# Performance work log

Hardware: AMD Instinct MI355X
Metric: run time of the kernel (lower is better)

The kernel has to match this reference:

```python
import jax, jax.numpy as jnp
import numpy as np

B, C, L, H = 4, 1024, 2048, 16
D = C // H


def setup_inputs() -> dict:
    key = jax.random.key(0)
    k1, k2, k3, k4 = jax.random.split(key, 4)
    queries = jax.random.normal(k1, (B, C, L), dtype=jnp.float32)
    mask = jax.random.randint(k2, (B, L), 0, 2, dtype=jnp.int32)
    # Conv1d(kernel_size=1, bias=False) weights, stored as [out_ch, in_ch]
    Wm = jax.random.normal(k3, (2 * C, C), dtype=jnp.float32) * (1.0 / np.sqrt(C))
    Wq = jax.random.normal(k4, (C, C), dtype=jnp.float32) * (1.0 / np.sqrt(C))
    return {"queries": queries, "mask": mask, "Wm": Wm, "Wq": Wq}


def reference(queries, mask, Wm, Wq):
    # 1x1 conv == channel-wise linear: [B,C,L] -> [B,L,out]
    mem = jnp.einsum("oc,bcl->blo", Wm, queries)   # [B, L, 2C]
    q = jnp.einsum("oc,bcl->blo", Wq, queries)      # [B, L, C]

    def split_heads(x):  # [B, L, C'] -> [B, H, L, D']
        b, l, c = x.shape
        return x.reshape(b, l, H, c // H).transpose(0, 2, 1, 3)

    Q = split_heads(q) * (D ** -0.5)                # [B, H, L, D]
    K = split_heads(mem[..., :C])                   # [B, H, L, D]
    V = split_heads(mem[..., C:])                   # [B, H, L, D]

    logits = jnp.einsum("bhqd,bhkd->bhqk", Q, K)    # [B, H, L, L]
    m = mask.astype(jnp.float32)[:, None, None, :]  # [B, 1, 1, L]
    NEG_INF = jnp.float32(-1e30)
    logits = logits * m + (1.0 - m) * NEG_INF
    weights = jax.nn.softmax(logits, axis=-1)
    x = jnp.einsum("bhqk,bhkd->bhqd", weights, V)   # [B, H, L, D]
    # combine heads and return [B, C, L]
    out = x.transpose(0, 2, 1, 3).reshape(B, L, C).transpose(0, 2, 1)
    return out
```

## Files before the change

### kernel.cpp

```cpp
#include <hip/hip_runtime.h>


typedef __bf16 bf16x8 __attribute__((ext_vector_type(8)));
typedef float f32x4 __attribute__((ext_vector_type(4)));
typedef float f32x16 __attribute__((ext_vector_type(16)));
typedef unsigned int u32x4 __attribute__((ext_vector_type(4)));

#define MFMA16(a, b, c) __builtin_amdgcn_mfma_f32_16x16x32_bf16((a), (b), (c), 0, 0, 0)
#define MFMA32(a, b, c) __builtin_amdgcn_mfma_f32_32x32x16_bf16((a), (b), (c), 0, 0, 0)

__device__ __forceinline__ unsigned short f2bf(float f) {
  unsigned int u = __float_as_uint(f);
  u += 0x7FFFu + ((u >> 16) & 1u);
  return (unsigned short)(u >> 16);
}

__device__ __forceinline__ void gload16(const void* g, void* lds) {
  __builtin_amdgcn_global_load_lds(
      (const __attribute__((address_space(1))) unsigned int*)g,
      (__attribute__((address_space(3))) unsigned int*)lds, 16, 0, 0);
}


__global__ __launch_bounds__(256) void castw_kernel(const float* __restrict__ Wm,
                                                    const float* __restrict__ Wq,
                                                    unsigned short* __restrict__ Wb) {
  size_t i = ((size_t)blockIdx.x * 256 + threadIdx.x) * 4;
  float4 v;
  if (i < (size_t)2048 * 1024) {
    v = *(const float4*)(Wm + i);
  } else {
    v = *(const float4*)(Wq + (i - (size_t)2048 * 1024));
    const float sc = 0.125f * 1.4426950408889634f;
    v.x *= sc; v.y *= sc; v.z *= sc; v.w *= sc;
  }
  ushort4 o;
  o.x = f2bf(v.x); o.y = f2bf(v.y); o.z = f2bf(v.z); o.w = f2bf(v.w);
  *(ushort4*)(Wb + i) = o;
}

__global__ __launch_bounds__(256) void transq_kernel(const float* __restrict__ q,
                                                     unsigned short* __restrict__ qT) {
  __shared__ float tile[32][33];
  int b = blockIdx.z;
  int l0 = blockIdx.x * 32, c0 = blockIdx.y * 32;
  int tx = threadIdx.x, ty = threadIdx.y;
  const float* src = q + ((size_t)b * 1024 + c0) * 2048 + l0;
#pragma unroll
  for (int i = 0; i < 4; i++)
    tile[ty + i * 8][tx] = src[(size_t)(ty + i * 8) * 2048 + tx];
  __syncthreads();
  unsigned short* dst = qT + ((size_t)b * 2048 + l0) * 1024 + c0;
#pragma unroll
  for (int i = 0; i < 4; i++)
    dst[(size_t)(ty + i * 8) * 1024 + tx] = f2bf(tile[tx][ty + i * 8]);
}

__global__ __launch_bounds__(256) void maskword_kernel(const int* __restrict__ mask,
                                                       unsigned int* __restrict__ mword) {
  int i = blockIdx.x * 256 + threadIdx.x;
  if (i < 4096) {
    const int* mp = mask + i * 2;
    mword[i] = (mp[0] ? 0xFFFFu : 0u) | (mp[1] ? 0xFFFF0000u : 0u);
  }
}


__global__ __launch_bounds__(256) void gemm_kernel(const unsigned short* __restrict__ Wb,
                                                   const unsigned short* __restrict__ qT,
                                                   unsigned short* __restrict__ Kb,
                                                   unsigned short* __restrict__ Vb,
                                                   unsigned short* __restrict__ Qb) {
  __shared__ __align__(16) unsigned short At[128 * 32];
  __shared__ __align__(16) unsigned short Bt[128 * 32];
  int n = blockIdx.x + 16 * (blockIdx.y + 24 * blockIdx.z);
  int lb = (n & 7) * 192 + (n >> 3);
  int bx = lb & 15;
  int by = (lb >> 4) % 24;
  int b = lb / 384;
  int o0 = by * 128, l0 = bx * 128;
  int tid = threadIdx.x, lane = tid & 63, wid = tid >> 6;
  int wr = wid >> 1, wc = wid & 1;
  int ln = lane & 15, g = lane >> 4;

  f32x4 acc[4][4];
#pragma unroll
  for (int m2 = 0; m2 < 4; m2++)
#pragma unroll
    for (int n2 = 0; n2 < 4; n2++) acc[m2][n2] = (f32x4){0.f, 0.f, 0.f, 0.f};

  const unsigned short* wsrc = Wb + (size_t)o0 * 1024;
  const unsigned short* xsrc = qT + ((size_t)b * 2048 + l0) * 1024;
  int c0 = tid, c1 = 256 + tid;

  for (int kk = 0; kk < 1024; kk += 32) {
    gload16(wsrc + (size_t)(c0 >> 2) * 1024 + kk + (c0 & 3) * 8, (char*)At + (size_t)wid * 1024);
    gload16(wsrc + (size_t)(c1 >> 2) * 1024 + kk + (c1 & 3) * 8, (char*)At + 4096 + (size_t)wid * 1024);
    gload16(xsrc + (size_t)(c0 >> 2) * 1024 + kk + (c0 & 3) * 8, (char*)Bt + (size_t)wid * 1024);
    gload16(xsrc + (size_t)(c1 >> 2) * 1024 + kk + (c1 & 3) * 8, (char*)Bt + 4096 + (size_t)wid * 1024);
    __syncthreads();
    bf16x8 af[4], bfv[4];
#pragma unroll
    for (int m2 = 0; m2 < 4; m2++)
      af[m2] = *(const bf16x8*)&At[(wr * 64 + m2 * 16 + ln) * 32 + g * 8];
#pragma unroll
    for (int n2 = 0; n2 < 4; n2++)
      bfv[n2] = *(const bf16x8*)&Bt[(wc * 64 + n2 * 16 + ln) * 32 + g * 8];
#pragma unroll
    for (int m2 = 0; m2 < 4; m2++)
#pragma unroll
      for (int n2 = 0; n2 < 4; n2++)
        acc[m2][n2] = MFMA16(af[m2], bfv[n2], acc[m2][n2]);
    __syncthreads();
  }

  int region = o0 >> 10;
#pragma unroll
  for (int m2 = 0; m2 < 4; m2++) {
    int orow = o0 + wr * 64 + m2 * 16 + g * 4;
#pragma unroll
    for (int n2 = 0; n2 < 4; n2++) {
      int l = l0 + wc * 64 + n2 * 16 + ln;
      if (region == 0) {
        int h = orow >> 6, d = orow & 63;
        ushort4 pk;
        pk.x = f2bf(acc[m2][n2][0]); pk.y = f2bf(acc[m2][n2][1]);
        pk.z = f2bf(acc[m2][n2][2]); pk.w = f2bf(acc[m2][n2][3]);
        *(ushort4*)&Kb[(((size_t)b * 16 + h) * 2048 + l) * 64 + d] = pk;
      } else if (region == 1) {
        int o2 = orow - 1024;
        int h = o2 >> 6, d = o2 & 63;
#pragma unroll
        for (int r = 0; r < 4; r++)
          Vb[(((size_t)b * 16 + h) * 64 + (d + r)) * 2048 + l] = f2bf(acc[m2][n2][r]);
      } else {
        int o2 = orow - 2048;
        int h = o2 >> 6, d = o2 & 63;
        ushort4 pk;
        pk.x = f2bf(acc[m2][n2][0]); pk.y = f2bf(acc[m2][n2][1]);
        pk.z = f2bf(acc[m2][n2][2]); pk.w = f2bf(acc[m2][n2][3]);
        *(ushort4*)&Qb[(((size_t)b * 16 + h) * 2048 + l) * 64 + d] = pk;
      }
    }
  }
}


__global__ __launch_bounds__(256) void attn_kernel(const unsigned short* __restrict__ Kb,
                                                   const unsigned short* __restrict__ Vb,
                                                   const unsigned short* __restrict__ Qb,
                                                   const unsigned int* __restrict__ mword,
                                                   float* __restrict__ out) {
  __shared__ __align__(16) unsigned short Kt[2][4096];
  __shared__ __align__(16) unsigned short Vt[2][4096];

  int n = blockIdx.x;
  int lb = (n & 7) * 128 + (n >> 3);
  int qt = lb & 15;
  int bh = lb >> 4;
  int b = bh >> 4, h = bh & 15;
  int tid = threadIdx.x, lane = tid & 63, w = tid >> 6;
  int c = lane & 31, hi = lane >> 5;
  int q0 = qt * 128 + w * 32;

  const unsigned short* Kp = Kb + (size_t)bh * 2048 * 64;
  const unsigned short* Vp = Vb + (size_t)bh * 2048 * 64;
  const unsigned short* Qp = Qb + (size_t)bh * 2048 * 64;
  const unsigned int* mwp = mword + b * 1024;

  bf16x8 qf[4];
#pragma unroll
  for (int ks = 0; ks < 4; ks++)
    qf[ks] = *(const bf16x8*)&Qp[(size_t)(q0 + c) * 64 + ks * 16 + hi * 8];

  f32x16 Ov0, Ov1, Os;
#pragma unroll
  for (int i = 0; i < 16; i++) { Ov0[i] = 0.f; Ov1[i] = 0.f; Os[i] = 0.f; }

  unsigned int ow = (c == 0) ? 0x3F803F80u : 0u;
  u32x4 ow4 = {ow, ow, ow, ow};
  bf16x8 bones = __builtin_bit_cast(bf16x8, ow4);

  int l8 = (lane & 7) * 16, l3 = lane >> 3;
  int cswz = (c & 7) << 4;

#pragma unroll
  for (int i = 0; i < 2; i++) {
    int widx = w * 2 + i;
    int row = widx * 8 + l3;
    int sb = l8 ^ ((row & 7) << 4);
    gload16((const char*)Kp + (size_t)row * 128 + sb, (char*)Kt[0] + widx * 1024);
    gload16((const char*)Vp + (size_t)row * 4096 + sb, (char*)Vt[0] + widx * 1024);
  }
  __syncthreads();

  for (int kb = 0; kb < 32; kb++) {
    int bs = kb & 1;
    if (kb < 31) {
#pragma unroll
      for (int i = 0; i < 2; i++) {
        int widx = w * 2 + i;
        int row = widx * 8 + l3;
        int sb = l8 ^ ((row & 7) << 4);
        gload16((const char*)Kp + (size_t)(kb * 64 + 64 + row) * 128 + sb,
                (char*)Kt[bs ^ 1] + widx * 1024);
        gload16((const char*)Vp + (size_t)row * 4096 + (kb + 1) * 128 + sb,
                (char*)Vt[bs ^ 1] + widx * 1024);
      }
    }
    u32x4 mw[4];
#pragma unroll
    for (int ks2 = 0; ks2 < 4; ks2++)
      mw[ks2] = *(const u32x4*)(mwp + kb * 32 + ks2 * 8 + hi * 4);

    f32x16 s0, s1;
#pragma unroll
    for (int i = 0; i < 16; i++) { s0[i] = 0.f; s1[i] = 0.f; }
    const char* Kbuf = (const char*)Kt[bs];
    __builtin_amdgcn_s_setprio(1);
#pragma unroll
    for (int ks = 0; ks < 4; ks++) {
      int off = (ks * 32 + hi * 16) ^ cswz;
      bf16x8 a0 = *(const bf16x8*)(Kbuf + c * 128 + off);
      bf16x8 a1 = *(const bf16x8*)(Kbuf + (c + 32) * 128 + off);
      s0 = MFMA32(a0, qf[ks], s0);
      s1 = MFMA32(a1, qf[ks], s1);
    }
    __builtin_amdgcn_s_setprio(0);
#pragma unroll
    for (int i = 0; i < 16; i++) {
      asm("v_exp_f32 %0, %1" : "=v"(s0[i]) : "v"(s0[i]));
      asm("v_exp_f32 %0, %1" : "=v"(s1[i]) : "v"(s1[i]));
    }
    bf16x8 pa[4];
#pragma unroll
    for (int ks2 = 0; ks2 < 4; ks2++) {
      int k1 = (ks2 & 1) * 8;
      unsigned int wds[4];
#pragma unroll
      for (int jj = 0; jj < 2; jj++) {
        unsigned int U, W;
        float u0 = (ks2 < 2) ? s0[k1 + 2 * jj] : s1[k1 + 2 * jj];
        float u1 = (ks2 < 2) ? s0[k1 + 2 * jj + 1] : s1[k1 + 2 * jj + 1];
        float w0 = (ks2 < 2) ? s0[k1 + 4 + 2 * jj] : s1[k1 + 4 + 2 * jj];
        float w1 = (ks2 < 2) ? s0[k1 + 5 + 2 * jj] : s1[k1 + 5 + 2 * jj];
        asm("v_cvt_pk_bf16_f32 %0, %1, %2" : "=v"(U) : "v"(u0), "v"(u1));
        asm("v_cvt_pk_bf16_f32 %0, %1, %2" : "=v"(W) : "v"(w0), "v"(w1));
        asm("v_permlane32_swap_b32 %0, %1" : "+v"(U), "+v"(W));
        wds[jj] = U;
        wds[2 + jj] = W;
      }
      u32x4 wv = {wds[0] & mw[ks2][0], wds[1] & mw[ks2][1],
                  wds[2] & mw[ks2][2], wds[3] & mw[ks2][3]};
      pa[ks2] = __builtin_bit_cast(bf16x8, wv);
    }
    const char* Vbuf = (const char*)Vt[bs];
    __builtin_amdgcn_s_setprio(1);
#pragma unroll
    for (int ks2 = 0; ks2 < 4; ks2++) {
      int off = (ks2 * 32 + hi * 16) ^ cswz;
      bf16x8 v0 = *(const bf16x8*)(Vbuf + c * 128 + off);
      bf16x8 v1 = *(const bf16x8*)(Vbuf + (c + 32) * 128 + off);
      Ov0 = MFMA32(pa[ks2], v0, Ov0);
      Ov1 = MFMA32(pa[ks2], v1, Ov1);
      Os = MFMA32(pa[ks2], bones, Os);
    }
    __builtin_amdgcn_s_setprio(0);
    __syncthreads();
  }

  float rinv[16];
#pragma unroll
  for (int r = 0; r < 16; r++) {
    float d0 = __int_as_float(__builtin_amdgcn_readlane(__float_as_int(Os[r]), 0));
    float d1 = __int_as_float(__builtin_amdgcn_readlane(__float_as_int(Os[r]), 32));
    rinv[r] = __builtin_amdgcn_rcpf(hi ? d1 : d0);
  }

  size_t obase = ((size_t)b * 1024 + h * 64) * 2048 + q0;
#pragma unroll
  for (int g2 = 0; g2 < 4; g2++) {
    int lq = g2 * 8 + hi * 4;
    float4 x0, x1;
    x0.x = Ov0[g2 * 4 + 0] * rinv[g2 * 4 + 0]; x0.y = Ov0[g2 * 4 + 1] * rinv[g2 * 4 + 1];
    x0.z = Ov0[g2 * 4 + 2] * rinv[g2 * 4 + 2]; x0.w = Ov0[g2 * 4 + 3] * rinv[g2 * 4 + 3];
    x1.x = Ov1[g2 * 4 + 0] * rinv[g2 * 4 + 0]; x1.y = Ov1[g2 * 4 + 1] * rinv[g2 * 4 + 1];
    x1.z = Ov1[g2 * 4 + 2] * rinv[g2 * 4 + 2]; x1.w = Ov1[g2 * 4 + 3] * rinv[g2 * 4 + 3];
    *(float4*)(out + obase + (size_t)c * 2048 + lq) = x0;
    *(float4*)(out + obase + (size_t)(32 + c) * 2048 + lq) = x1;
  }
}

extern "C" void kernel_launch(void* const* d_in, const int* in_sizes, int n_in,
                              void* d_out, int out_size, void* d_ws, size_t ws_size,
                              hipStream_t stream) {
  const float* queries = (const float*)d_in[0];
  const int* mask = (const int*)d_in[1];
  const float* Wm = (const float*)d_in[2];
  const float* Wq = (const float*)d_in[3];
  float* out = (float*)d_out;

  char* ws = (char*)d_ws;
  unsigned short* Wb = (unsigned short*)(ws);
  unsigned short* qT = (unsigned short*)(ws + 6291456);
  unsigned short* Kb = (unsigned short*)(ws + 23068672);
  unsigned short* Vb = (unsigned short*)(ws + 39845888);
  unsigned short* Qb = (unsigned short*)(ws + 56623104);
  unsigned int* mwp = (unsigned int*)(ws + 73400320);

  castw_kernel<<<3072, 256, 0, stream>>>(Wm, Wq, Wb);
  transq_kernel<<<dim3(64, 32, 4), dim3(32, 8), 0, stream>>>(queries, qT);
  maskword_kernel<<<16, 256, 0, stream>>>(mask, mwp);
  gemm_kernel<<<dim3(16, 24, 4), 256, 0, stream>>>(Wb, qT, Kb, Vb, Qb);
  attn_kernel<<<1024, 256, 0, stream>>>(Kb, Vb, Qb, mwp, out);
}
```

Baseline: 261.9 us.

## Double-buffer GEMM LDS tiles and stage attention mask in LDS

The projection GEMM gets double-buffered LDS tiles, prefetching the next K-slice while the current one runs through MFMA. Explicit s_barrier and vmcnt waits replace __syncthreads in both GEMM and attention loops. The attention kernel now preloads the per-batch mask words into LDS once instead of reading global memory every iteration, and the score accumulators start from a zero operand rather than being cleared. Hand-written waitcnt and barrier placement depends on the exact count of outstanding loads, so a miscount could cause races.

```diff
diff --git a/kernel.cpp b/kernel.cpp
--- a/kernel.cpp
+++ b/kernel.cpp
@@ -71,8 +71,8 @@
                                                    unsigned short* __restrict__ Kb,
                                                    unsigned short* __restrict__ Vb,
                                                    unsigned short* __restrict__ Qb) {
-  __shared__ __align__(16) unsigned short At[128 * 32];
-  __shared__ __align__(16) unsigned short Bt[128 * 32];
+  __shared__ __align__(16) unsigned short At[2][4096];
+  __shared__ __align__(16) unsigned short Bt[2][4096];
   int n = blockIdx.x + 16 * (blockIdx.y + 24 * blockIdx.z);
   int lb = (n & 7) * 192 + (n >> 3);
   int bx = lb & 15;
@@ -93,25 +93,45 @@
   const unsigned short* xsrc = qT + ((size_t)b * 2048 + l0) * 1024;
   int c0 = tid, c1 = 256 + tid;
 
-  for (int kk = 0; kk < 1024; kk += 32) {
-    gload16(wsrc + (size_t)(c0 >> 2) * 1024 + kk + (c0 & 3) * 8, (char*)At + (size_t)wid * 1024);
-    gload16(wsrc + (size_t)(c1 >> 2) * 1024 + kk + (c1 & 3) * 8, (char*)At + 4096 + (size_t)wid * 1024);
-    gload16(xsrc + (size_t)(c0 >> 2) * 1024 + kk + (c0 & 3) * 8, (char*)Bt + (size_t)wid * 1024);
-    gload16(xsrc + (size_t)(c1 >> 2) * 1024 + kk + (c1 & 3) * 8, (char*)Bt + 4096 + (size_t)wid * 1024);
-    __syncthreads();
+  {
+    int kk = 0;
+    gload16(wsrc + (size_t)(c0 >> 2) * 1024 + kk + (c0 & 3) * 8, (char*)At[0] + (size_t)wid * 1024);
+    gload16(wsrc + (size_t)(c1 >> 2) * 1024 + kk + (c1 & 3) * 8, (char*)At[0] + 4096 + (size_t)wid * 1024);
+    gload16(xsrc + (size_t)(c0 >> 2) * 1024 + kk + (c0 & 3) * 8, (char*)Bt[0] + (size_t)wid * 1024);
+    gload16(xsrc + (size_t)(c1 >> 2) * 1024 + kk + (c1 & 3) * 8, (char*)Bt[0] + 4096 + (size_t)wid * 1024);
+  }
+
+  for (int t = 0; t < 32; t++) {
+    int bs = t & 1;
+    __builtin_amdgcn_sched_barrier(0);
+    asm volatile("s_barrier" ::: "memory");
+    if (t < 31) {
+      int kk = (t + 1) * 32;
+      gload16(wsrc + (size_t)(c0 >> 2) * 1024 + kk + (c0 & 3) * 8, (char*)At[bs ^ 1] + (size_t)wid * 1024);
+      gload16(wsrc + (size_t)(c1 >> 2) * 1024 + kk + (c1 & 3) * 8, (char*)At[bs ^ 1] + 4096 + (size_t)wid * 1024);
+      gload16(xsrc + (size_t)(c0 >> 2) * 1024 + kk + (c0 & 3) * 8, (char*)Bt[bs ^ 1] + (size_t)wid * 1024);
+      gload16(xsrc + (size_t)(c1 >> 2) * 1024 + kk + (c1 & 3) * 8, (char*)Bt[bs ^ 1] + 4096 + (size_t)wid * 1024);
+      asm volatile("s_waitcnt vmcnt(4)" ::: "memory");
+    } else {
+      asm volatile("s_waitcnt vmcnt(0)" ::: "memory");
+    }
+    asm volatile("s_barrier" ::: "memory");
+    __builtin_amdgcn_sched_barrier(0);
+
     bf16x8 af[4], bfv[4];
 #pragma unroll
     for (int m2 = 0; m2 < 4; m2++)
-      af[m2] = *(const bf16x8*)&At[(wr * 64 + m2 * 16 + ln) * 32 + g * 8];
+      af[m2] = *(const bf16x8*)&At[bs][(wr * 64 + m2 * 16 + ln) * 32 + g * 8];
 #pragma unroll
     for (int n2 = 0; n2 < 4; n2++)
-      bfv[n2] = *(const bf16x8*)&Bt[(wc * 64 + n2 * 16 + ln) * 32 + g * 8];
+      bfv[n2] = *(const bf16x8*)&Bt[bs][(wc * 64 + n2 * 16 + ln) * 32 + g * 8];
+    __builtin_amdgcn_s_setprio(1);
 #pragma unroll
     for (int m2 = 0; m2 < 4; m2++)
 #pragma unroll
       for (int n2 = 0; n2 < 4; n2++)
         acc[m2][n2] = MFMA16(af[m2], bfv[n2], acc[m2][n2]);
-    __syncthreads();
+    __builtin_amdgcn_s_setprio(0);
   }
 
   int region = o0 >> 10;
@@ -153,6 +173,7 @@
                                                    float* __restrict__ out) {
   __shared__ __align__(16) unsigned short Kt[2][4096];
   __shared__ __align__(16) unsigned short Vt[2][4096];
+  __shared__ __align__(16) unsigned int Mt[1024];
 
   int n = blockIdx.x;
   int lb = (n & 7) * 128 + (n >> 3);
@@ -173,9 +194,10 @@
   for (int ks = 0; ks < 4; ks++)
     qf[ks] = *(const bf16x8*)&Qp[(size_t)(q0 + c) * 64 + ks * 16 + hi * 8];
 
-  f32x16 Ov0, Ov1, Os;
-#pragma unroll
-  for (int i = 0; i < 16; i++) { Ov0[i] = 0.f; Ov1[i] = 0.f; Os[i] = 0.f; }
+  f32x16 fz;
+#pragma unroll
+  for (int i = 0; i < 16; i++) fz[i] = 0.f;
+  f32x16 Ov0 = fz, Ov1 = fz, Os = fz;
 
   unsigned int ow = (c == 0) ? 0x3F803F80u : 0u;
   u32x4 ow4 = {ow, ow, ow, ow};
@@ -192,10 +214,12 @@
     gload16((const char*)Kp + (size_t)row * 128 + sb, (char*)Kt[0] + widx * 1024);
     gload16((const char*)Vp + (size_t)row * 4096 + sb, (char*)Vt[0] + widx * 1024);
   }
-  __syncthreads();
+  gload16((const char*)mwp + (size_t)w * 1024 + (size_t)lane * 16, (char*)Mt + w * 1024);
 
   for (int kb = 0; kb < 32; kb++) {
     int bs = kb & 1;
+    __builtin_amdgcn_sched_barrier(0);
+    asm volatile("s_barrier" ::: "memory");
     if (kb < 31) {
 #pragma unroll
       for (int i = 0; i < 2; i++) {
@@ -207,15 +231,19 @@
         gload16((const char*)Vp + (size_t)row * 4096 + (kb + 1) * 128 + sb,
                 (char*)Vt[bs ^ 1] + widx * 1024);
       }
-    }
+      asm volatile("s_waitcnt vmcnt(4)" ::: "memory");
+    } else {
+      asm volatile("s_waitcnt vmcnt(0)" ::: "memory");
+    }
+    asm volatile("s_barrier" ::: "memory");
+    __builtin_amdgcn_sched_barrier(0);
+
     u32x4 mw[4];
 #pragma unroll
     for (int ks2 = 0; ks2 < 4; ks2++)
-      mw[ks2] = *(const u32x4*)(mwp + kb * 32 + ks2 * 8 + hi * 4);
+      mw[ks2] = *(const u32x4*)((const char*)Mt + kb * 128 + ks2 * 32 + hi * 16);
 
     f32x16 s0, s1;
-#pragma unroll
-    for (int i = 0; i < 16; i++) { s0[i] = 0.f; s1[i] = 0.f; }
     const char* Kbuf = (const char*)Kt[bs];
     __builtin_amdgcn_s_setprio(1);
 #pragma unroll
@@ -223,8 +251,13 @@
       int off = (ks * 32 + hi * 16) ^ cswz;
       bf16x8 a0 = *(const bf16x8*)(Kbuf + c * 128 + off);
       bf16x8 a1 = *(const bf16x8*)(Kbuf + (c + 32) * 128 + off);
-      s0 = MFMA32(a0, qf[ks], s0);
-      s1 = MFMA32(a1, qf[ks], s1);
+      if (ks == 0) {
+        s0 = MFMA32(a0, qf[0], fz);
+        s1 = MFMA32(a1, qf[0], fz);
+      } else {
+        s0 = MFMA32(a0, qf[ks], s0);
+        s1 = MFMA32(a1, qf[ks], s1);
+      }
     }
     __builtin_amdgcn_s_setprio(0);
 #pragma unroll
@@ -266,7 +299,6 @@
       Os = MFMA32(pa[ks2], bones, Os);
     }
     __builtin_amdgcn_s_setprio(0);
-    __syncthreads();
   }
 
   float rinv[16];
```

New measurement: 266.3 us. Within noise of the previous version (+1.7%).
